# Kernel tuning notes

Measured on AMD Instinct MI355X. Metric: run time of the kernel, lower is better.

Reference implementation:

```python
import jax, jax.numpy as jnp
import numpy as np

B, C, H_RES, W_RES = 8, 192, 64, 64


def dwconv(x, kern, pad):
    # depthwise conv, x: (B,C,H,W), kern: (C,1,k,k)
    return jax.lax.conv_general_dilated(
        x, kern, window_strides=(1, 1), padding=[(pad, pad), (pad, pad)],
        dimension_numbers=('NCHW', 'OIHW', 'NCHW'),
        feature_group_count=x.shape[1])


def omni_shift(x, alpha, dw1, dw3, dw5):
    # OmniShift (training branch): learnable mix of identity + depthwise 1x1/3x3/5x5
    return (alpha[0] * x + alpha[1] * dwconv(x, dw1, 0)
            + alpha[2] * dwconv(x, dw3, 1) + alpha[3] * dwconv(x, dw5, 2))


def biwkv(w, u, k, v):
    # Bidirectional WKV (Vision-RWKV style):
    # out_t = (sum_{i!=t} e^{-(|t-i|-1)w + k_i} v_i + e^{u+k_t} v_t)
    #       / (sum_{i!=t} e^{-(|t-i|-1)w + k_i}       + e^{u+k_t})
    # w,u: (C,); k,v: (B,T,C). Implemented as two stable log-scaled scans.
    kT = jnp.moveaxis(k, 1, 0)  # (T,B,C)
    vT = jnp.moveaxis(v, 1, 0)
    bc = (k.shape[0], k.shape[2])
    init = (jnp.full(bc, -jnp.inf, k.dtype), jnp.zeros(bc, k.dtype), jnp.zeros(bc, k.dtype))

    def step(carry, inp):
        p, num, den = carry          # state = e^p * (num, den) over strictly-previous tokens
        kt, vt = inp
        out = (p, num, den)          # emit BEFORE absorbing token t (i != t term)
        q = jnp.maximum(p - w, kt)
        e1 = jnp.exp(p - w - q)
        e2 = jnp.exp(kt - q)
        return (q, e1 * num + e2 * vt, e1 * den + e2), out

    _, (pf, nf, df) = jax.lax.scan(step, init, (kT, vT))
    _, (pb, nb, db) = jax.lax.scan(step, init, (kT[::-1], vT[::-1]))
    pb, nb, db = pb[::-1], nb[::-1], db[::-1]

    ps = u + kT                      # self term exponent
    r = jnp.maximum(jnp.maximum(pf, pb), ps)
    ef, eb, es = jnp.exp(pf - r), jnp.exp(pb - r), jnp.exp(ps - r)
    out = (ef * nf + eb * nb + es * vT) / (ef * df + eb * db + es)
    return jnp.moveaxis(out, 0, 1)   # (B,T,C)


def setup_inputs() -> dict:
    key = jax.random.key(0)
    ks = jax.random.split(key, 12)
    s = 1.0 / np.sqrt(C)
    inp = {
        'x': jax.random.normal(ks[0], (B, C, H_RES, W_RES), jnp.float32),
        'w_key': jax.random.normal(ks[1], (C, C), jnp.float32) * s,
        'w_value': jax.random.normal(ks[2], (C, C), jnp.float32) * s,
        'w_recept': jax.random.normal(ks[3], (C, C), jnp.float32) * s,
        'w_out': jax.random.normal(ks[4], (C, C), jnp.float32) * s,
        'decay': jax.random.normal(ks[5], (C,), jnp.float32),
        'boost': jax.random.normal(ks[6], (C,), jnp.float32),
        'alpha': jax.random.normal(ks[7], (4,), jnp.float32),
        'dw1': jax.random.normal(ks[8], (C, 1, 1, 1), jnp.float32) * s,
        'dw3': jax.random.normal(ks[9], (C, 1, 3, 3), jnp.float32) * (s / 3.0),
        'dw5': jax.random.normal(ks[10], (C, 1, 5, 5), jnp.float32) * (s / 5.0),
        'H': H_RES,
        'W': W_RES,
    }
    return inp


def reference(x, w_key, w_value, w_recept, w_out, decay, boost, alpha, dw1, dw3, dw5, H, W):
    Bn, Cn = x.shape[0], x.shape[1]
    T = H * W
    xs = omni_shift(x, alpha, dw1, dw3, dw5)                 # (B,C,H,W)
    xt = jnp.transpose(xs.reshape(Bn, Cn, T), (0, 2, 1))     # (B,T,C)
    k = jnp.einsum('btc,dc->btd', xt, w_key)
    v = jnp.einsum('btc,dc->btd', xt, w_value)
    sr = jax.nn.sigmoid(jnp.einsum('btc,dc->btd', xt, w_recept))
    y = biwkv(decay / T, boost / T, k, v)                    # (B,T,C)
    y = sr * y
    y = jnp.einsum('btd,cd->btc', y, w_out)
    return jnp.transpose(y, (0, 2, 1)).reshape(Bn, Cn, H, W)
```

## Files before the change

kernel.cpp:

```cpp
#include <hip/hip_runtime.h>
#include <math.h>

#define Cn 192
#define Bn 8
#define Tn 4096
#define HW 64

typedef unsigned short u16;
typedef unsigned int u32;
typedef __attribute__((ext_vector_type(8))) __bf16 bf16x8;
typedef __attribute__((ext_vector_type(16))) float f32x16;

__device__ __forceinline__ void gload16(const void* g, void* l) {
    __builtin_amdgcn_global_load_lds(
        (const __attribute__((address_space(1))) void*)g,
        (__attribute__((address_space(3))) void*)l, 16, 0, 0);
}

__device__ __forceinline__ void split_bf16(float x, u16 &h, u16 &l) {
    u32 u = __float_as_uint(x);
    u32 uh = (u + 0x7FFFu + ((u >> 16) & 1u)) & 0xFFFF0000u;
    h = (u16)(uh >> 16);
    float r = x - __uint_as_float(uh);
    u32 ur = __float_as_uint(r);
    l = (u16)((ur + 0x7FFFu + ((ur >> 16) & 1u)) >> 16);
}

__global__ __launch_bounds__(256) void omni_kernel(const float* __restrict__ x,
                                                   const float* __restrict__ alpha,
                                                   const float* __restrict__ dw1,
                                                   const float* __restrict__ dw3,
                                                   const float* __restrict__ dw5,
                                                   const float* __restrict__ Wk,
                                                   const float* __restrict__ Wv,
                                                   const float* __restrict__ Wr,
                                                   const float* __restrict__ Wo,
                                                   u16* __restrict__ xhi,
                                                   u16* __restrict__ xlo,
                                                   u16* __restrict__ wh,
                                                   u16* __restrict__ wl) {
    const int tid = threadIdx.x;
    if (blockIdx.x >= 1536) {
        const int base = (blockIdx.x - 1536) * 768;
        #pragma unroll
        for (int jj = 0; jj < 3; ++jj) {
            int idx = base + jj * 256 + tid;
            int mat = idx / 36864;
            int off = idx - mat * 36864;
            const float* src = (mat == 0) ? Wk : (mat == 1) ? Wv : (mat == 2) ? Wr : Wo;
            u16 h, l;
            split_bf16(src[off], h, l);
            wh[idx] = h;
            wl[idx] = l;
        }
        return;
    }

    const int plane = blockIdx.x;
    const int c = plane % Cn;
    const float* xin = x + (size_t)plane * Tn;
    u16* oh = xhi + (size_t)plane * Tn;
    u16* ol = xlo + (size_t)plane * Tn;

    __shared__ float tile[68 * 68];
    __shared__ float wk[25];

    if (tid == 0) {
        const float a0 = alpha[0], a1 = alpha[1], a2 = alpha[2], a3 = alpha[3];
        #pragma unroll
        for (int j = 0; j < 25; ++j) wk[j] = a3 * dw5[c * 25 + j];
        #pragma unroll
        for (int dy = 0; dy < 3; ++dy)
            #pragma unroll
            for (int dx = 0; dx < 3; ++dx)
                wk[(dy + 1) * 5 + (dx + 1)] += a2 * dw3[c * 9 + dy * 3 + dx];
        wk[12] += a1 * dw1[c] + a0;
    }
    for (int i = tid; i < 68 * 68; i += 256) {
        int r = i / 68, cc = i - r * 68;
        int gy = r - 2, gx = cc - 2;
        float v = 0.f;
        if (gy >= 0 && gy < HW && gx >= 0 && gx < HW) v = xin[gy * HW + gx];
        tile[i] = v;
    }
    __syncthreads();

    const int py = tid >> 3;
    const int px0 = (tid & 7) << 3;

    #pragma unroll
    for (int half = 0; half < 2; ++half) {
        const int y = py + half * 32;
        float row[5][12];
        #pragma unroll
        for (int dy = 0; dy < 5; ++dy) {
            const float4* rp = (const float4*)&tile[(y + dy) * 68 + px0];
            float4 r0 = rp[0], r1 = rp[1], r2 = rp[2];
            row[dy][0] = r0.x; row[dy][1] = r0.y; row[dy][2]  = r0.z; row[dy][3]  = r0.w;
            row[dy][4] = r1.x; row[dy][5] = r1.y; row[dy][6]  = r1.z; row[dy][7]  = r1.w;
            row[dy][8] = r2.x; row[dy][9] = r2.y; row[dy][10] = r2.z; row[dy][11] = r2.w;
        }
        u32 ph[4], pl[4];
        #pragma unroll
        for (int jj = 0; jj < 8; ++jj) {
            float acc = 0.f;
            #pragma unroll
            for (int dy = 0; dy < 5; ++dy)
                #pragma unroll
                for (int dx = 0; dx < 5; ++dx)
                    acc = fmaf(row[dy][jj + dx], wk[dy * 5 + dx], acc);
            u16 h, l2;
            split_bf16(acc, h, l2);
            if (jj & 1) { ph[jj >> 1] |= ((u32)h) << 16; pl[jj >> 1] |= ((u32)l2) << 16; }
            else        { ph[jj >> 1] = h;               pl[jj >> 1] = l2; }
        }
        *(uint4*)&oh[y * 64 + px0] = make_uint4(ph[0], ph[1], ph[2], ph[3]);
        *(uint4*)&ol[y * 64 + px0] = make_uint4(pl[0], pl[1], pl[2], pl[3]);
    }
}

__global__ __launch_bounds__(256) void gemm_proj(const u16* __restrict__ wh,
                                                 const u16* __restrict__ wl,
                                                 const u16* __restrict__ Xh,
                                                 const u16* __restrict__ Xl,
                                                 float* __restrict__ O0,
                                                 float* __restrict__ O1,
                                                 float* __restrict__ O2) {
    __shared__ u16 Ah_[3 * 64 * 32], Al_[3 * 64 * 32];
    __shared__ u16 Bh_[128 * 36], Bl_[128 * 36];

    const int tid  = threadIdx.x;
    const int l    = tid & 63;
    const int wave = tid >> 6;
    const int wm   = wave >> 1, wn = wave & 1;
    const int m0   = blockIdx.y * 64;
    const int t0   = blockIdx.x * 128;
    const size_t xb = (size_t)blockIdx.z * Cn * Tn;
    const int cpair = tid & 15;
    const int toct  = tid >> 4;

    f32x16 acc[3][2];
    #pragma unroll
    for (int m = 0; m < 3; ++m)
        #pragma unroll
        for (int nf = 0; nf < 2; ++nf)
            #pragma unroll
            for (int r = 0; r < 16; ++r) acc[m][nf][r] = 0.f;

    uint4 rh0, rh1, rl0, rl1;

    auto loadB = [&](int k0) {
        size_t g = xb + (size_t)(k0 + 2 * cpair) * Tn + t0 + toct * 8;
        rh0 = *(const uint4*)&Xh[g];
        rh1 = *(const uint4*)&Xh[g + Tn];
        rl0 = *(const uint4*)&Xl[g];
        rl1 = *(const uint4*)&Xl[g + Tn];
    };
    auto writeB = [&]() {
        const u32 h0[4] = {rh0.x, rh0.y, rh0.z, rh0.w};
        const u32 h1[4] = {rh1.x, rh1.y, rh1.z, rh1.w};
        const u32 l0[4] = {rl0.x, rl0.y, rl0.z, rl0.w};
        const u32 l1[4] = {rl1.x, rl1.y, rl1.z, rl1.w};
        #pragma unroll
        for (int j = 0; j < 8; ++j) {
            int t = toct * 8 + j;
            int sh = 16 * (j & 1);
            u32 a = (h0[j >> 1] >> sh) & 0xFFFFu;
            u32 b = (h1[j >> 1] >> sh) & 0xFFFFu;
            *(u32*)&Bh_[t * 36 + 2 * cpair] = a | (b << 16);
            u32 c = (l0[j >> 1] >> sh) & 0xFFFFu;
            u32 d = (l1[j >> 1] >> sh) & 0xFFFFu;
            *(u32*)&Bl_[t * 36 + 2 * cpair] = c | (d << 16);
        }
    };
    auto stageA = [&](int k0) {
        #pragma unroll
        for (int i = 0; i < 3; ++i) {
            int idx = i * 256 + tid;
            int row = idx >> 2;
            int cb  = (idx & 3) ^ ((row >> 1) & 3);
            int grow = (row >> 6) * 192 + m0 + (row & 63);
            gload16(wh + (size_t)grow * Cn + k0 + cb * 8, Ah_ + idx * 8);
            gload16(wl + (size_t)grow * Cn + k0 + cb * 8, Al_ + idx * 8);
        }
    };
    auto compute = [&]() {
        #pragma unroll
        for (int kh = 0; kh < 2; ++kh) {
            const int cbb = kh * 2 + (l >> 5);
            bf16x8 ah[3], al[3];
            #pragma unroll
            for (int m = 0; m < 3; ++m) {
                int r = m * 64 + wm * 32 + (l & 31);
                int off = r * 32 + ((cbb ^ ((r >> 1) & 3)) << 3);
                ah[m] = *(const bf16x8*)&Ah_[off];
                al[m] = *(const bf16x8*)&Al_[off];
            }
            #pragma unroll
            for (int nf = 0; nf < 2; ++nf) {
                int t = wn * 64 + nf * 32 + (l & 31);
                int o = t * 36 + cbb * 8;
                union { uint2 q[2]; bf16x8 v; } th, tl2;
                th.q[0]  = *(const uint2*)&Bh_[o];
                th.q[1]  = *(const uint2*)&Bh_[o + 4];
                tl2.q[0] = *(const uint2*)&Bl_[o];
                tl2.q[1] = *(const uint2*)&Bl_[o + 4];
                #pragma unroll
                for (int m = 0; m < 3; ++m) {
                    acc[m][nf] = __builtin_amdgcn_mfma_f32_32x32x16_bf16(ah[m], th.v,  acc[m][nf], 0, 0, 0);
                    acc[m][nf] = __builtin_amdgcn_mfma_f32_32x32x16_bf16(ah[m], tl2.v, acc[m][nf], 0, 0, 0);
                    acc[m][nf] = __builtin_amdgcn_mfma_f32_32x32x16_bf16(al[m], th.v,  acc[m][nf], 0, 0, 0);
                }
            }
        }
    };

    loadB(0);
    stageA(0);
    writeB();
    __syncthreads();
    loadB(32);
    for (int ks = 0; ks < 6; ++ks) {
        compute();
        if (ks < 5) {
            __syncthreads();
            writeB();
            stageA((ks + 1) * 32);
            __syncthreads();
            if (ks < 4) loadB((ks + 2) * 32);
        }
    }

    float* Os[3] = {O0, O1, O2};
    #pragma unroll
    for (int m = 0; m < 3; ++m) {
        float* O = Os[m] + (size_t)blockIdx.z * Cn * Tn;
        #pragma unroll
        for (int nf = 0; nf < 2; ++nf) {
            int col = t0 + wn * 64 + nf * 32 + (l & 31);
            #pragma unroll
            for (int r = 0; r < 16; ++r) {
                int row = m0 + wm * 32 + (r & 3) + 8 * (r >> 2) + 4 * (l >> 5);
                O[(size_t)row * Tn + col] = acc[m][nf][r];
            }
        }
    }
}

__global__ __launch_bounds__(256) void wkv_stats(const float* __restrict__ kg,
                                                 const float* __restrict__ vg,
                                                 const float* __restrict__ decay,
                                                 float4* __restrict__ states) {
    const int row = blockIdx.x;
    const int d = row % Cn;
    const float* kr = kg + (size_t)row * Tn;
    const float* vr = vg + (size_t)row * Tn;

    const int tid = threadIdx.x;
    const int t0 = tid * 16;

    float kk[16], vv[16];
    #pragma unroll
    for (int j = 0; j < 16; j += 4) {
        *(float4*)&kk[j] = *(const float4*)&kr[t0 + j];
        *(float4*)&vv[j] = *(const float4*)&vr[t0 + j];
    }

    const float ww = decay[d] * (1.0f / (float)Tn);
    const float lam = expf(-ww);
    const float lam16 = expf(-16.0f * ww);

    float a[16];
    #pragma unroll
    for (int j = 0; j < 16; ++j) a[j] = expf(kk[j]);

    float SN = 0.f, SD = 0.f;
    #pragma unroll
    for (int j = 0; j < 16; ++j) { SN = fmaf(lam, SN, a[j] * vv[j]); SD = fmaf(lam, SD, a[j]); }
    float BN = 0.f, BD = 0.f;
    #pragma unroll
    for (int j = 15; j >= 0; --j) { BN = fmaf(lam, BN, a[j] * vv[j]); BD = fmaf(lam, BD, a[j]); }

    __shared__ float sN[2][256], sD[2][256];

    sN[0][tid] = SN; sD[0][tid] = SD;
    __syncthreads();
    int src = 0;
    float f = lam16;
    for (int o = 1; o < 256; o <<= 1) {
        float nN = sN[src][tid], nD = sD[src][tid];
        if (tid >= o) { nN = fmaf(f, sN[src][tid - o], nN); nD = fmaf(f, sD[src][tid - o], nD); }
        sN[src ^ 1][tid] = nN; sD[src ^ 1][tid] = nD;
        __syncthreads();
        src ^= 1; f = f * f;
    }
    const float CfN = (tid > 0) ? sN[src][tid - 1] : 0.f;
    const float CfD = (tid > 0) ? sD[src][tid - 1] : 0.f;
    __syncthreads();

    sN[0][tid] = BN; sD[0][tid] = BD;
    __syncthreads();
    src = 0; f = lam16;
    for (int o = 1; o < 256; o <<= 1) {
        float nN = sN[src][tid], nD = sD[src][tid];
        if (tid + o < 256) { nN = fmaf(f, sN[src][tid + o], nN); nD = fmaf(f, sD[src][tid + o], nD); }
        sN[src ^ 1][tid] = nN; sD[src ^ 1][tid] = nD;
        __syncthreads();
        src ^= 1; f = f * f;
    }
    const float CbN = (tid < 255) ? sN[src][tid + 1] : 0.f;
    const float CbD = (tid < 255) ? sD[src][tid + 1] : 0.f;

    const int b = row / Cn;
    states[((size_t)(b * 256 + tid)) * Cn + d] = make_float4(CfN, CfD, CbN, CbD);
}

__global__ __launch_bounds__(512) void wkv_out(const float* __restrict__ kb,
                                               const float* __restrict__ vb,
                                               const float* __restrict__ srl,
                                               const float4* __restrict__ states,
                                               const float* __restrict__ decay,
                                               const float* __restrict__ boost,
                                               const u16* __restrict__ wh,
                                               const u16* __restrict__ wl,
                                               float* __restrict__ out) {
    __shared__ u16 Yh_[128 * 196], Yl_[128 * 196];
    __shared__ u16 Ah_[192 * 32], Al_[192 * 32];

    const int tid = threadIdx.x;
    const int b = blockIdx.y;
    const int t0 = blockIdx.x * 128;

    for (int pass = 0; pass < 3; ++pass) {
        const int task = pass * 512 + tid;
        const int d  = task % Cn;
        const int ch = task / Cn;
        const size_t rbase = ((size_t)b * Cn + d) * Tn + t0 + ch * 16;
        const float4 st = states[((size_t)(b * 256 + (t0 >> 4) + ch)) * Cn + d];
        const float ww = decay[d] * (1.0f / (float)Tn);
        const float lam = expf(-ww);
        const float u = boost[d] * (1.0f / (float)Tn);

        float kk[16], vv[16], sl[16];
        #pragma unroll
        for (int j = 0; j < 16; j += 4) {
            *(float4*)&kk[j] = *(const float4*)&kb[rbase + j];
            *(float4*)&vv[j] = *(const float4*)&vb[rbase + j];
            *(float4*)&sl[j] = *(const float4*)&srl[rbase + j];
        }
        float a[16];
        #pragma unroll
        for (int j = 0; j < 16; ++j) a[j] = expf(kk[j]);

        float fN[16], fD[16];
        float cN = st.x, cD = st.y;
        #pragma unroll
        for (int j = 0; j < 16; ++j) {
            fN[j] = cN; fD[j] = cD;
            cN = fmaf(lam, cN, a[j] * vv[j]);
            cD = fmaf(lam, cD, a[j]);
        }
        float bN = st.z, bD = st.w;
        #pragma unroll
        for (int j = 15; j >= 0; --j) {
            const float es = expf(u + kk[j]);
            const float y = (fN[j] + bN + es * vv[j]) / (fD[j] + bD + es);
            const float sig = 1.0f / (1.0f + expf(-sl[j]));
            u16 h, l2;
            split_bf16(sig * y, h, l2);
            const int t = ch * 16 + j;
            Yh_[t * 196 + d] = h;
            Yl_[t * 196 + d] = l2;
            bN = fmaf(lam, bN, a[j] * vv[j]);
            bD = fmaf(lam, bD, a[j]);
        }
    }
    __syncthreads();

    const int l = tid & 63;
    const int wave = tid >> 6;
    const int wm = wave >> 2;
    const int wn = wave & 3;

    f32x16 acc[3];
    #pragma unroll
    for (int mf = 0; mf < 3; ++mf)
        #pragma unroll
        for (int r = 0; r < 16; ++r) acc[mf][r] = 0.f;

    for (int ks = 0; ks < 6; ++ks) {
        {
            int idx = tid;
            int row = idx >> 2;
            int cb = (idx & 3) ^ ((row >> 1) & 3);
            gload16(wh + (size_t)(576 + row) * Cn + ks * 32 + cb * 8, Ah_ + idx * 8);
            gload16(wl + (size_t)(576 + row) * Cn + ks * 32 + cb * 8, Al_ + idx * 8);
            if (tid < 256) {
                idx = 512 + tid;
                row = idx >> 2;
                cb = (idx & 3) ^ ((row >> 1) & 3);
                gload16(wh + (size_t)(576 + row) * Cn + ks * 32 + cb * 8, Ah_ + idx * 8);
                gload16(wl + (size_t)(576 + row) * Cn + ks * 32 + cb * 8, Al_ + idx * 8);
            }
        }
        __syncthreads();
        #pragma unroll
        for (int kh = 0; kh < 2; ++kh) {
            const int cbb = kh * 2 + (l >> 5);
            bf16x8 ah[3], al[3];
            #pragma unroll
            for (int mf = 0; mf < 3; ++mf) {
                int r = wm * 96 + mf * 32 + (l & 31);
                int off = r * 32 + ((cbb ^ ((r >> 1) & 3)) << 3);
                ah[mf] = *(const bf16x8*)&Ah_[off];
                al[mf] = *(const bf16x8*)&Al_[off];
            }
            const int t = wn * 32 + (l & 31);
            const int o = t * 196 + ks * 32 + cbb * 8;
            union { uint2 q[2]; bf16x8 v; } bh, bl;
            bh.q[0] = *(const uint2*)&Yh_[o];
            bh.q[1] = *(const uint2*)&Yh_[o + 4];
            bl.q[0] = *(const uint2*)&Yl_[o];
            bl.q[1] = *(const uint2*)&Yl_[o + 4];
            #pragma unroll
            for (int mf = 0; mf < 3; ++mf) {
                acc[mf] = __builtin_amdgcn_mfma_f32_32x32x16_bf16(ah[mf], bh.v, acc[mf], 0, 0, 0);
                acc[mf] = __builtin_amdgcn_mfma_f32_32x32x16_bf16(ah[mf], bl.v, acc[mf], 0, 0, 0);
                acc[mf] = __builtin_amdgcn_mfma_f32_32x32x16_bf16(al[mf], bh.v, acc[mf], 0, 0, 0);
            }
        }
        __syncthreads();
    }

    #pragma unroll
    for (int mf = 0; mf < 3; ++mf) {
        const int col = t0 + wn * 32 + (l & 31);
        #pragma unroll
        for (int r = 0; r < 16; ++r) {
            int row = wm * 96 + mf * 32 + (r & 3) + 8 * (r >> 2) + 4 * (l >> 5);
            out[((size_t)b * Cn + row) * Tn + col] = acc[mf][r];
        }
    }
}

extern "C" void kernel_launch(void* const* d_in, const int* in_sizes, int n_in,
                              void* d_out, int out_size, void* d_ws, size_t ws_size,
                              hipStream_t stream) {
    const float* x        = (const float*)d_in[0];
    const float* w_key    = (const float*)d_in[1];
    const float* w_value  = (const float*)d_in[2];
    const float* w_recept = (const float*)d_in[3];
    const float* w_out    = (const float*)d_in[4];
    const float* decay    = (const float*)d_in[5];
    const float* boost    = (const float*)d_in[6];
    const float* alpha    = (const float*)d_in[7];
    const float* dw1      = (const float*)d_in[8];
    const float* dw3      = (const float*)d_in[9];
    const float* dw5      = (const float*)d_in[10];

    const size_t S = (size_t)Bn * Cn * Tn;
    u16* R0 = (u16*)d_ws;
    u16* R1 = R0 + 2 * S;
    u16* R2 = R1 + 2 * S;
    u16* whp = R2 + 2 * S;
    u16* wlp = whp + 4 * 36864;

    u16* xs_hi = R0;        u16* xs_lo = R0 + S;
    float* kb  = (float*)R1;
    float* vb  = (float*)R2;
    float* srl = (float*)d_out;
    float4* states = (float4*)R0;
    float* out = (float*)d_out;

    omni_kernel<<<dim3(1536 + 192), 256, 0, stream>>>(x, alpha, dw1, dw3, dw5,
                                                      w_key, w_value, w_recept, w_out,
                                                      xs_hi, xs_lo, whp, wlp);

    gemm_proj<<<dim3(32, 3, 8), 256, 0, stream>>>(whp, wlp, xs_hi, xs_lo, kb, vb, srl);

    wkv_stats<<<dim3(Bn * Cn), 256, 0, stream>>>(kb, vb, decay, states);

    wkv_out<<<dim3(32, 8), 512, 0, stream>>>(kb, vb, srl, states, decay, boost,
                                             whp, wlp, out);
}
```

Measured before the change: 107.9 us.

## Fuse per-chunk WKV partial sums into projection GEMM epilogue

After: 110.6 us. 1.03x slower.

```diff
diff --git a/kernel.cpp b/kernel.cpp
--- a/kernel.cpp
+++ b/kernel.cpp
@@ -125,9 +125,16 @@
                                                  const u16* __restrict__ Xl,
                                                  float* __restrict__ O0,
                                                  float* __restrict__ O1,
-                                                 float* __restrict__ O2) {
-    __shared__ u16 Ah_[3 * 64 * 32], Al_[3 * 64 * 32];
-    __shared__ u16 Bh_[128 * 36], Bl_[128 * 36];
+                                                 float* __restrict__ O2,
+                                                 const float* __restrict__ decay,
+                                                 float4* __restrict__ sums) {
+    __shared__ __align__(16) char pool_[43008];
+    u16* Ah_ = (u16*)pool_;
+    u16* Al_ = (u16*)(pool_ + 12288);
+    u16* Bh_ = (u16*)(pool_ + 24576);
+    u16* Bl_ = (u16*)(pool_ + 33792);
+    float* kS = (float*)pool_;
+    float* vS = (float*)(pool_ + 17152);
 
     const int tid  = threadIdx.x;
     const int l    = tid & 63;
@@ -245,45 +252,55 @@
             }
         }
     }
-}
-
-__global__ __launch_bounds__(256) void wkv_stats(const float* __restrict__ kg,
-                                                 const float* __restrict__ vg,
-                                                 const float* __restrict__ decay,
-                                                 float4* __restrict__ states) {
+
+    const float lamS = expf(-decay[m0 + (tid & 63)] * (1.0f / (float)Tn));
+    #pragma unroll
+    for (int ph = 0; ph < 2; ++ph) {
+        __syncthreads();
+        #pragma unroll
+        for (int r = 0; r < 16; ++r) {
+            int drow = wm * 32 + (r & 3) + 8 * (r >> 2) + 4 * (l >> 5);
+            int tc   = wn * 32 + (l & 31);
+            kS[drow * 67 + tc] = acc[0][ph][r];
+            vS[drow * 67 + tc] = acc[1][ph][r];
+        }
+        __syncthreads();
+        {
+            const int d_local = tid & 63;
+            const int ch = tid >> 6;
+            const float* kr = &kS[d_local * 67 + ch * 16];
+            const float* vr = &vS[d_local * 67 + ch * 16];
+            float aa[16], av[16];
+            #pragma unroll
+            for (int j = 0; j < 16; ++j) { aa[j] = expf(kr[j]); av[j] = aa[j] * vr[j]; }
+            float SN = 0.f, SD = 0.f;
+            #pragma unroll
+            for (int j = 0; j < 16; ++j) { SN = fmaf(lamS, SN, av[j]); SD = fmaf(lamS, SD, aa[j]); }
+            float BN = 0.f, BD = 0.f;
+            #pragma unroll
+            for (int j = 15; j >= 0; --j) { BN = fmaf(lamS, BN, av[j]); BD = fmaf(lamS, BD, aa[j]); }
+            int chG = (t0 >> 4) + (ch >> 1) * 4 + ph * 2 + (ch & 1);
+            sums[((size_t)(blockIdx.z * 256 + chG)) * Cn + (m0 + d_local)] =
+                make_float4(SN, SD, BN, BD);
+        }
+    }
+}
+
+__global__ __launch_bounds__(256) void wkv_scan(const float4* __restrict__ sums,
+                                                const float* __restrict__ decay,
+                                                float4* __restrict__ states) {
     const int row = blockIdx.x;
     const int d = row % Cn;
-    const float* kr = kg + (size_t)row * Tn;
-    const float* vr = vg + (size_t)row * Tn;
-
+    const int b = row / Cn;
     const int tid = threadIdx.x;
-    const int t0 = tid * 16;
-
-    float kk[16], vv[16];
-    #pragma unroll
-    for (int j = 0; j < 16; j += 4) {
-        *(float4*)&kk[j] = *(const float4*)&kr[t0 + j];
-        *(float4*)&vv[j] = *(const float4*)&vr[t0 + j];
-    }
-
+
+    const float4 s = sums[((size_t)(b * 256 + tid)) * Cn + d];
     const float ww = decay[d] * (1.0f / (float)Tn);
-    const float lam = expf(-ww);
     const float lam16 = expf(-16.0f * ww);
 
-    float a[16];
-    #pragma unroll
-    for (int j = 0; j < 16; ++j) a[j] = expf(kk[j]);
-
-    float SN = 0.f, SD = 0.f;
-    #pragma unroll
-    for (int j = 0; j < 16; ++j) { SN = fmaf(lam, SN, a[j] * vv[j]); SD = fmaf(lam, SD, a[j]); }
-    float BN = 0.f, BD = 0.f;
-    #pragma unroll
-    for (int j = 15; j >= 0; --j) { BN = fmaf(lam, BN, a[j] * vv[j]); BD = fmaf(lam, BD, a[j]); }
-
     __shared__ float sN[2][256], sD[2][256];
 
-    sN[0][tid] = SN; sD[0][tid] = SD;
+    sN[0][tid] = s.x; sD[0][tid] = s.y;
     __syncthreads();
     int src = 0;
     float f = lam16;
@@ -298,7 +315,7 @@
     const float CfD = (tid > 0) ? sD[src][tid - 1] : 0.f;
     __syncthreads();
 
-    sN[0][tid] = BN; sD[0][tid] = BD;
+    sN[0][tid] = s.z; sD[0][tid] = s.w;
     __syncthreads();
     src = 0; f = lam16;
     for (int o = 1; o < 256; o <<= 1) {
@@ -311,7 +328,6 @@
     const float CbN = (tid < 255) ? sN[src][tid + 1] : 0.f;
     const float CbD = (tid < 255) ? sD[src][tid + 1] : 0.f;
 
-    const int b = row / Cn;
     states[((size_t)(b * 256 + tid)) * Cn + d] = make_float4(CfN, CfD, CbN, CbD);
 }
 
@@ -469,6 +485,7 @@
     float* kb  = (float*)R1;
     float* vb  = (float*)R2;
     float* srl = (float*)d_out;
+    float4* sums = (float4*)(wlp + 4 * 36864);
     float4* states = (float4*)R0;
     float* out = (float*)d_out;
 
@@ -476,9 +493,10 @@
                                                       w_key, w_value, w_recept, w_out,
                                                       xs_hi, xs_lo, whp, wlp);
 
-    gemm_proj<<<dim3(32, 3, 8), 256, 0, stream>>>(whp, wlp, xs_hi, xs_lo, kb, vb, srl);
-
-    wkv_stats<<<dim3(Bn * Cn), 256, 0, stream>>>(kb, vb, decay, states);
+    gemm_proj<<<dim3(32, 3, 8), 256, 0, stream>>>(whp, wlp, xs_hi, xs_lo, kb, vb, srl,
+                                                  decay, sums);
+
+    wkv_scan<<<dim3(Bn * Cn), 256, 0, stream>>>(sums, decay, states);
 
     wkv_out<<<dim3(32, 8), 512, 0, stream>>>(kb, vb, srl, states, decay, boost,
                                              whp, wlp, out);
```
